# Performance work log

Hardware: AMD Instinct MI355X
Metric: run time of the kernel (lower is better)

## Reference

```python
import jax, jax.numpy as jnp
import numpy as np


def pairwise_distance(x):
    # x: [B,N,F] -> squared euclidean distance matrix [B,N,N]
    sq = jnp.sum(x * x, axis=-1)
    d = sq[:, :, None] + sq[:, None, :] - 2.0 * jnp.einsum('bnd,bmd->bnm', x, x)
    return jnp.maximum(d, 0.0)


def knn_adjacency(dist, k):
    # keep the k nearest neighbors of each point (binary adjacency)
    B, N, _ = dist.shape
    idx = jax.lax.top_k(-dist, k)[1]  # [B,N,k]
    A = jnp.zeros((B, N, N), dist.dtype)
    return A.at[jnp.arange(B)[:, None, None], jnp.arange(N)[None, :, None], idx].set(1.0)


def get_laplacian(A):
    # normalized graph Laplacian L = I - D^{-1/2} A D^{-1/2}
    d = jnp.sum(A, axis=-1)
    dinv = jnp.where(d > 0, 1.0 / jnp.sqrt(jnp.maximum(d, 1e-12)), 0.0)
    An = A * dinv[:, :, None] * dinv[:, None, :]
    return jnp.eye(A.shape[-1], dtype=A.dtype)[None] - An


def cheb_conv(x, L, W, b, K):
    # DenseChebConv: Chebyshev recurrence T0=x, T1=Lx, Tk=2L T_{k-1}-T_{k-2};
    # concat along features then dense projection. x:[B,N,Fin], W:[K*Fin,Fout]
    xs = [x]
    if K > 1:
        xs.append(jnp.einsum('bnm,bmf->bnf', L, x))
    for _ in range(2, K):
        xs.append(2.0 * jnp.einsum('bnm,bmf->bnf', L, xs[-1]) - xs[-2])
    xk = jnp.concatenate(xs, axis=-1)
    return jnp.einsum('bnf,fo->bno', xk, W) + b


def segment_max(out, idx):
    # fused replacement of the per-batch/per-cluster python loops:
    # out:[B,N,F], idx:[B,R,S] -> max-pooled cluster features [B,R,F]
    B = out.shape[0]
    g = out[jnp.arange(B)[:, None, None], idx]  # [B,R,S,F]
    return jnp.max(g, axis=2)


def setup_inputs():
    key = jax.random.key(0)
    ks = jax.random.split(key, 12)
    B, N, R, S, P = 32, 1024, 64, 16, 55
    inp = {}
    inp['x'] = jax.random.normal(ks[0], (B, N, 7), jnp.float32)
    inp['x2'] = jax.random.normal(ks[1], (B, N, 3), jnp.float32)
    inp['laplacian_Reeb'] = jax.random.normal(ks[2], (B, R, R), jnp.float32)
    inp['W1'] = jax.random.normal(ks[3], (3 * 7, 64), jnp.float32) * 0.1
    inp['b1'] = jnp.zeros((64,), jnp.float32)
    inp['W_reeb'] = jax.random.normal(ks[4], (6 * 64, 256), jnp.float32) * 0.05
    inp['b_reeb'] = jnp.zeros((256,), jnp.float32)
    inp['W_fps'] = jax.random.normal(ks[5], (6 * 64, 256), jnp.float32) * 0.05
    inp['b_fps'] = jnp.zeros((256,), jnp.float32)
    inp['fc1_w'] = jax.random.normal(ks[6], (512, 256), jnp.float32) * 0.05
    inp['fc1_b'] = jnp.zeros((256,), jnp.float32)
    inp['fc3_w'] = jax.random.normal(ks[7], (256, 40), jnp.float32) * 0.05
    inp['fc3_b'] = jnp.zeros((40,), jnp.float32)
    inp['sccs'] = jax.random.randint(ks[8], (B, R, S), 0, N)
    inp['sccs_fps'] = jax.random.randint(ks[9], (B, P, N), 0, N)
    inp['k'] = 30
    inp['batch_size'] = B
    inp['num_points'] = N
    return inp


def reference(x, x2, laplacian_Reeb, W1, b1, W_reeb, b_reeb, W_fps, b_fps,
              fc1_w, fc1_b, fc3_w, fc3_b, sccs, sccs_fps, k, batch_size, num_points):
    sg = jax.lax.stop_gradient
    # point-cloud kNN Laplacian (torch.no_grad in original)
    L = sg(get_laplacian(knn_adjacency(pairwise_distance(x), k)))
    out = jax.nn.relu(cheb_conv(x, L, W1, b1, 3))  # [B,N,64]
    reg1 = jnp.sum(jnp.einsum('bnf,bnm,bmg->bfg', out, L, out) ** 2)
    # Reeb-graph segment max pooling (no_grad in original)
    V_reeb = sg(segment_max(out, sccs))  # [B,R,64]
    L_reeb = sg(laplacian_Reeb)
    out_reeb = jax.nn.relu(cheb_conv(V_reeb, L_reeb, W_reeb, b_reeb, 6))  # [B,R,256]
    reg2 = jnp.sum(jnp.einsum('bnf,bnm,bmg->bfg', out_reeb, L_reeb, out_reeb) ** 2)
    # FPS cluster max pooling (no_grad in original)
    V_fps = sg(segment_max(out, sccs_fps))  # [B,55,64]
    L_fps = sg(get_laplacian(pairwise_distance(V_fps)))
    out_fps = jax.nn.relu(cheb_conv(V_fps, L_fps, W_fps, b_fps, 6))  # [B,55,256]
    reg3 = jnp.sum(jnp.einsum('bnf,bnm,bmg->bfg', out_fps, L_fps, out_fps) ** 2)
    feat = jnp.concatenate([jnp.max(out_reeb, axis=1), jnp.max(out_fps, axis=1)], axis=1)  # [B,512]
    h = jax.nn.relu(feat @ fc1_w + fc1_b)
    logits = h @ fc3_w + fc3_b  # [B,40]
    regs = jnp.stack([reg1, reg2, reg3,
                      jnp.sum(fc1_w[:, 0] ** 2), fc1_b[0] ** 2,
                      jnp.sum(fc3_w[:, 0] ** 2), fc3_b[0] ** 2])
    return logits, regs
```

## Files before the change

### kernel.cpp

```cpp
#include <hip/hip_runtime.h>
#include <math.h>

#define BN 32
#define NP 1024
#define KNN 30
#define NR 64
#define NFPS 55

__device__ __forceinline__ float lap_s() {
    const float dv = 1.0f / sqrtf(30.0f);
    return dv * dv;
}

__device__ __forceinline__ float dist7(const float4& xiA, const float4& xiB,
                                       float sqi, const float4& ca, const float4& cb) {
#pragma clang fp contract(off)
    float dot = xiA.x * ca.x;
    dot = fmaf(xiA.y, ca.y, dot);
    dot = fmaf(xiA.z, ca.z, dot);
    dot = fmaf(xiA.w, ca.w, dot);
    dot = fmaf(xiB.x, cb.x, dot);
    dot = fmaf(xiB.y, cb.y, dot);
    dot = fmaf(xiB.z, cb.z, dot);
    float r = sqi + cb.w;
    r = r - 2.f * dot;
    return fmaxf(r, 0.f);
}

__global__ __launch_bounds__(256) void k_knn(const float* __restrict__ x,
                                             int* __restrict__ knn,
                                             float* __restrict__ xs1,
                                             const float* __restrict__ fc1_w,
                                             const float* __restrict__ fc1_b,
                                             const float* __restrict__ fc3_w,
                                             const float* __restrict__ fc3_b,
                                             float* __restrict__ regs) {
    __shared__ float xls[NP * 8];
    __shared__ float vals[4 * KNN * 64];
    __shared__ float Tm[4 * 64];
    __shared__ int   Pk[4 * 64];
    int b = blockIdx.x;
    int t = threadIdx.x;
    int ln = t & 63, wv = t >> 6;

    if (b == 0 && blockIdx.y == 0) {
        float* r1 = vals;
        float* r2 = vals + 256;
        float s1 = 0.f;
        for (int i = t; i < 512; i += 256) { float v = fc1_w[(size_t)i * 256]; s1 += v * v; }
        float v2 = fc3_w[(size_t)t * 40];
        r1[t] = s1; r2[t] = v2 * v2;
        __syncthreads();
        for (int st = 128; st > 0; st >>= 1) {
            if (t < st) { r1[t] += r1[t + st]; r2[t] += r2[t + st]; }
            __syncthreads();
        }
        if (t == 0) {
            regs[0] = 0.f; regs[1] = 0.f; regs[2] = 0.f;
            regs[3] = r1[0];
            regs[4] = fc1_b[0] * fc1_b[0];
            regs[5] = r2[0];
            regs[6] = fc3_b[0] * fc3_b[0];
        }
        __syncthreads();
    }

    const float* xb = x + (size_t)b * NP * 7;
    for (int q = t; q < NP * 8; q += 256) {
        int r = q >> 3, d = q & 7;
        xls[q] = (d < 7) ? xb[r * 7 + d] : 0.f;
    }
    __syncthreads();
    for (int r = t; r < NP; r += 256) {
        float s = 0.f;
#pragma unroll
        for (int d = 0; d < 7; ++d) { float v = xls[r * 8 + d]; s += v * v; }
        xls[r * 8 + 7] = s;
    }
    __syncthreads();

    int grow = blockIdx.y * 64 + ln;
    float4 xiA = *(const float4*)&xls[grow * 8];
    float4 xiB = *(const float4*)&xls[grow * 8 + 4];
    float sqi = xiB.w;

    float bd[KNN];
#pragma unroll
    for (int q = 0; q < KNN; ++q) bd[q] = __builtin_inff();
    int jbase = wv * 256;
    for (int jc = 0; jc < 256; jc += 4) {
        const float* p = &xls[(jbase + jc) * 8];
        float4 a0 = *(const float4*)(p +  0), b0 = *(const float4*)(p +  4);
        float4 a1 = *(const float4*)(p +  8), b1 = *(const float4*)(p + 12);
        float4 a2 = *(const float4*)(p + 16), b2 = *(const float4*)(p + 20);
        float4 a3 = *(const float4*)(p + 24), b3 = *(const float4*)(p + 28);
        float d0 = dist7(xiA, xiB, sqi, a0, b0);
        float d1 = dist7(xiA, xiB, sqi, a1, b1);
        float d2 = dist7(xiA, xiB, sqi, a2, b2);
        float d3 = dist7(xiA, xiB, sqi, a3, b3);
#pragma unroll
        for (int q = KNN - 1; q >= 1; --q) bd[q] = __builtin_amdgcn_fmed3f(bd[q - 1], d0, bd[q]);
        bd[0] = fminf(bd[0], d0);
#pragma unroll
        for (int q = KNN - 1; q >= 1; --q) bd[q] = __builtin_amdgcn_fmed3f(bd[q - 1], d1, bd[q]);
        bd[0] = fminf(bd[0], d1);
#pragma unroll
        for (int q = KNN - 1; q >= 1; --q) bd[q] = __builtin_amdgcn_fmed3f(bd[q - 1], d2, bd[q]);
        bd[0] = fminf(bd[0], d2);
#pragma unroll
        for (int q = KNN - 1; q >= 1; --q) bd[q] = __builtin_amdgcn_fmed3f(bd[q - 1], d3, bd[q]);
        bd[0] = fminf(bd[0], d3);
    }
#pragma unroll
    for (int q = 0; q < KNN; ++q) vals[wv * (KNN * 64) + q * 64 + ln] = bd[q];
    __syncthreads();

    if (t < 64) {
        const float inf = __builtin_inff();
        float h0 = vals[0 * 1920 + t];
        float h1 = vals[1 * 1920 + t];
        float h2 = vals[2 * 1920 + t];
        float h3 = vals[3 * 1920 + t];
        int p0 = 0, p1 = 0, p2 = 0, p3 = 0;
        for (int s = 0; s < KNN; ++s) {
            float best = h0; int bw = 0;
            if (h1 < best) { best = h1; bw = 1; }
            if (h2 < best) { best = h2; bw = 2; }
            if (h3 < best) { best = h3; bw = 3; }
            if (bw == 0)      { ++p0; h0 = (p0 < KNN) ? vals[0 * 1920 + p0 * 64 + t] : inf; }
            else if (bw == 1) { ++p1; h1 = (p1 < KNN) ? vals[1 * 1920 + p1 * 64 + t] : inf; }
            else if (bw == 2) { ++p2; h2 = (p2 < KNN) ? vals[2 * 1920 + p2 * 64 + t] : inf; }
            else              { ++p3; h3 = (p3 < KNN) ? vals[3 * 1920 + p3 * 64 + t] : inf; }
        }
        int bacc = 0;
        int tks[4] = {p0, p1, p2, p3};
#pragma unroll
        for (int w = 0; w < 4; ++w) {
            int tk = tks[w];
            float T; int need;
            if (tk == 0) { T = -__builtin_inff(); need = 0; }
            else {
                T = vals[w * 1920 + (tk - 1) * 64 + t];
                need = 1;
                for (int q = tk - 2; q >= 0; --q) {
                    if (vals[w * 1920 + q * 64 + t] == T) ++need; else break;
                }
            }
            Tm[w * 64 + t] = T;
            Pk[w * 64 + t] = bacc | (need << 8) | (tk << 16);
            bacc += tk;
        }
    }
    __syncthreads();

    float Tw = Tm[wv * 64 + ln];
    int pk = Pk[wv * 64 + ln];
    int base = pk & 255, need = (pk >> 8) & 255, tk = pk >> 16;
    int* kout = knn + ((size_t)b * NP + grow) * KNN;
    float n0 = 0.f, n1 = 0.f, n2 = 0.f, n3 = 0.f, n4 = 0.f, n5 = 0.f, n6 = 0.f;
    int cs = 0, ct = 0;
    for (int jc = 0; jc < 256; jc += 4) {
        const float* p = &xls[(jbase + jc) * 8];
        float4 a0 = *(const float4*)(p +  0), b0 = *(const float4*)(p +  4);
        float4 a1 = *(const float4*)(p +  8), b1 = *(const float4*)(p + 12);
        float4 a2 = *(const float4*)(p + 16), b2 = *(const float4*)(p + 20);
        float4 a3 = *(const float4*)(p + 24), b3 = *(const float4*)(p + 28);
        float d0 = dist7(xiA, xiB, sqi, a0, b0);
        float d1 = dist7(xiA, xiB, sqi, a1, b1);
        float d2 = dist7(xiA, xiB, sqi, a2, b2);
        float d3 = dist7(xiA, xiB, sqi, a3, b3);
#pragma unroll
        for (int u = 0; u < 4; ++u) {
            float dist = (u == 0) ? d0 : (u == 1) ? d1 : (u == 2) ? d2 : d3;
            const float4& ca = (u == 0) ? a0 : (u == 1) ? a1 : (u == 2) ? a2 : a3;
            const float4& cb = (u == 0) ? b0 : (u == 1) ? b1 : (u == 2) ? b2 : b3;
            bool lt = dist < Tw;
            bool eq = (dist == Tw) && (ct < need);
            if ((lt || eq) && (cs + ct < tk)) {
                kout[base + cs + ct] = jbase + jc + u;
                cs += lt ? 1 : 0;
                ct += eq ? 1 : 0;
                n0 += ca.x; n1 += ca.y; n2 += ca.z; n3 += ca.w;
                n4 += cb.x; n5 += cb.y; n6 += cb.z;
            }
        }
    }
    for (int q = cs + ct; q < tk; ++q) kout[base + q] = grow;
    float* nsb = vals;
    nsb[wv * 448 + 0 * 64 + ln] = n0;
    nsb[wv * 448 + 1 * 64 + ln] = n1;
    nsb[wv * 448 + 2 * 64 + ln] = n2;
    nsb[wv * 448 + 3 * 64 + ln] = n3;
    nsb[wv * 448 + 4 * 64 + ln] = n4;
    nsb[wv * 448 + 5 * 64 + ln] = n5;
    nsb[wv * 448 + 6 * 64 + ln] = n6;
    __syncthreads();
    for (int u = t; u < 448; u += 256) {
        int d = u >> 6, rl = u & 63;
        float tot = nsb[d * 64 + rl] + nsb[448 + d * 64 + rl]
                  + nsb[896 + d * 64 + rl] + nsb[1344 + d * 64 + rl];
        int gr = blockIdx.y * 64 + rl;
        xs1[((size_t)b * NP + gr) * 7 + d] = xls[gr * 8 + d] - lap_s() * tot;
    }
}

__global__ __launch_bounds__(256) void k_out(const float* __restrict__ x,
                                             const float* __restrict__ xs1,
                                             const int* __restrict__ knn,
                                             const float* __restrict__ W1,
                                             const float* __restrict__ b1,
                                             float* __restrict__ out) {
    __shared__ float x1s[NP * 7];
    __shared__ float x0s[128 * 7];
    __shared__ float fr[128 * 21];
    __shared__ float W1s[21 * 64];
    __shared__ float b1s[64];
    int b = blockIdx.x;
    int rbase = blockIdx.y * 128;
    int t = threadIdx.x;
    for (int q = t; q < NP * 7; q += 256) x1s[q] = xs1[(size_t)b * NP * 7 + q];
    for (int q = t; q < 128 * 7; q += 256) x0s[q] = x[(size_t)b * NP * 7 + (size_t)rbase * 7 + q];
    for (int q = t; q < 21 * 64; q += 256) W1s[q] = W1[q];
    if (t < 64) b1s[t] = b1[t];
    __syncthreads();
    if (t < 128) {
        int i = rbase + t;
        float f[21];
#pragma unroll
        for (int d = 0; d < 7; ++d) { f[d] = x0s[t * 7 + d]; f[7 + d] = x1s[i * 7 + d]; }
        float ns[7] = {0.f, 0.f, 0.f, 0.f, 0.f, 0.f, 0.f};
        const int* kn = knn + ((size_t)b * NP + i) * KNN;
        for (int q = 0; q < KNN; ++q) {
            int j = kn[q];
#pragma unroll
            for (int d = 0; d < 7; ++d) ns[d] += x1s[j * 7 + d];
        }
        const float s = lap_s();
#pragma unroll
        for (int d = 0; d < 7; ++d) f[14 + d] = 2.f * (f[7 + d] - s * ns[d]) - f[d];
#pragma unroll
        for (int d = 0; d < 21; ++d) fr[t * 21 + d] = f[d];
    }
    __syncthreads();
    int o = t & 63, g = t >> 6;
    for (int m = 0; m < 32; ++m) {
        int r = g * 32 + m;
        float acc = b1s[o];
#pragma unroll
        for (int d = 0; d < 21; ++d) acc += fr[r * 21 + d] * W1s[d * 64 + o];
        out[((size_t)b * NP + rbase + r) * 64 + o] = fmaxf(acc, 0.f);
    }
}

__global__ __launch_bounds__(256) void k_z1v(const float* __restrict__ out,
                                             const int* __restrict__ knn,
                                             const int* __restrict__ sccs,
                                             const int* __restrict__ sccs_fps,
                                             float* __restrict__ Z1,
                                             float* __restrict__ Vr,
                                             float* __restrict__ Vf) {
    __shared__ int idxs[1024];
    __shared__ float red[256];
    int b = blockIdx.x, y = blockIdx.y;
    int t = threadIdx.x;
    const float* ob = out + (size_t)b * NP * 64;
    if (y < 256) {
        int i = y * 4 + (t >> 6);
        int f = t & 63;
        const int* kn = knn + ((size_t)b * NP + i) * KNN;
        float sum = 0.f;
        for (int q = 0; q < KNN; ++q) sum += ob[(size_t)kn[q] * 64 + f];
        Z1[((size_t)b * NP + i) * 64 + f] = ob[(size_t)i * 64 + f] - lap_s() * sum;
    } else if (y < 272) {
        int r = (y - 256) * 4 + (t >> 6);
        int f = t & 63;
        const int* sc = sccs + ((size_t)b * NR + r) * 16;
        float m = -__builtin_inff();
        for (int q = 0; q < 16; ++q) m = fmaxf(m, ob[(size_t)sc[q] * 64 + f]);
        Vr[((size_t)b * NR + r) * 64 + f] = m;
    } else {
        int p = y - 272;
        const int* sp = sccs_fps + ((size_t)b * NFPS + p) * 1024;
        for (int q = t; q < 1024; q += 256) idxs[q] = sp[q];
        __syncthreads();
        int f = t & 63, sc = t >> 6;
        float m = -__builtin_inff();
        for (int s = sc; s < 1024; s += 4) m = fmaxf(m, ob[(size_t)idxs[s] * 64 + f]);
        red[t] = m; __syncthreads();
        if (sc == 0) {
            m = fmaxf(fmaxf(red[f], red[64 + f]), fmaxf(red[128 + f], red[192 + f]));
            Vf[((size_t)b * NFPS + p) * 64 + f] = m;
        }
    }
}

__global__ __launch_bounds__(256) void k_t1_lfps(const float* __restrict__ out,
                                                 const float* __restrict__ Z1,
                                                 const float* __restrict__ Vfps,
                                                 float* __restrict__ regs,
                                                 float* __restrict__ Lf) {
    __shared__ float buf[8448];
    int b = blockIdx.x, y = blockIdx.y;
    int t = threadIdx.x;
    if (y < 2) {
        float* os = buf;
        float* zs = buf + 4096;
        float* red = buf + 8192;
        int f0 = y * 32;
        int fl = t >> 3;
        int gb = (t & 7) * 8;
        float acc[8];
#pragma unroll
        for (int q = 0; q < 8; ++q) acc[q] = 0.f;
        for (int c = 0; c < 16; ++c) {
            const float* ob = out + ((size_t)b * NP + c * 64) * 64;
            const float* zb = Z1 + ((size_t)b * NP + c * 64) * 64;
            for (int q = t; q < 64 * 64; q += 256) { os[q] = ob[q]; zs[q] = zb[q]; }
            __syncthreads();
            for (int n = 0; n < 64; ++n) {
                float a = os[n * 64 + f0 + fl];
#pragma unroll
                for (int q = 0; q < 8; ++q) acc[q] += a * zs[n * 64 + gb + q];
            }
            __syncthreads();
        }
        float loc = 0.f;
#pragma unroll
        for (int q = 0; q < 8; ++q) loc += acc[q] * acc[q];
        red[t] = loc; __syncthreads();
        for (int st = 128; st > 0; st >>= 1) { if (t < st) red[t] += red[t + st]; __syncthreads(); }
        if (t == 0) atomicAdd(&regs[0], red[0]);
    } else {
        float* Vs = buf;
        float* sq = buf + 3520;
        float* dist = buf + 3584;
        float* dinv = buf + 6609;
        for (int q = t; q < NFPS * 64; q += 256) Vs[q] = Vfps[(size_t)b * NFPS * 64 + q];
        __syncthreads();
        if (t < NFPS) {
            float s = 0.f;
            for (int f = 0; f < 64; ++f) { float v = Vs[t * 64 + f]; s += v * v; }
            sq[t] = s;
        }
        __syncthreads();
        for (int q = t; q < NFPS * NFPS; q += 256) {
            int i = q / NFPS, j = q % NFPS;
            float dot = 0.f;
            for (int f = 0; f < 64; ++f) dot += Vs[i * 64 + f] * Vs[j * 64 + f];
            dist[q] = fmaxf(sq[i] + sq[j] - 2.f * dot, 0.f);
        }
        __syncthreads();
        if (t < NFPS) {
            float s = 0.f;
            for (int j = 0; j < NFPS; ++j) s += dist[t * NFPS + j];
            dinv[t] = (s > 0.f) ? 1.0f / sqrtf(fmaxf(s, 1e-12f)) : 0.f;
        }
        __syncthreads();
        for (int q = t; q < NFPS * NFPS; q += 256) {
            int i = q / NFPS, j = q % NFPS;
            Lf[(size_t)b * NFPS * NFPS + q] = ((i == j) ? 1.f : 0.f) - dist[q] * dinv[i] * dinv[j];
        }
    }
}

template<int N>
__device__ __forceinline__ void cheb_impl(const float* __restrict__ L,
                                          const float* __restrict__ V,
                                          const float* __restrict__ W,
                                          const float* __restrict__ bias,
                                          float* __restrict__ out,
                                          float* __restrict__ Z,
                                          float* Ls, float* bA, float* bB, float* Ws,
                                          int b, int sl) {
    constexpr int NPAD = (N + 3) & ~3;
    int t = threadIdx.x;
    int c0 = (t & 15) * 4;
    int r0 = (t >> 4) * 4;

    for (int q = t; q < 64 * 64; q += 256) { Ls[q] = 0.f; bA[q] = 0.f; bB[q] = 0.f; }
    __syncthreads();
    for (int q = t; q < N * N; q += 256) {
        int r = q / N, m = q % N;
        Ls[r * 64 + m] = L[(size_t)b * N * N + q];
    }
    for (int q = t; q < N * 64; q += 256) bA[q] = V[(size_t)b * N * 64 + q];
    {
        const float* Wk = W + sl * 64;
        for (int q = t; q < 64 * 64; q += 256) Ws[q] = Wk[(q >> 6) * 256 + (q & 63)];
    }
    float4 a4[4];
    {
        float4 bv = *(const float4*)&bias[sl * 64 + c0];
#pragma unroll
        for (int i = 0; i < 4; ++i) a4[i] = bv;
    }
    __syncthreads();

    auto accum = [&](const float* xb) {
#pragma unroll 2
        for (int m = 0; m < 64; m += 4) {
            float4 xv[4], wv[4];
#pragma unroll
            for (int i = 0; i < 4; ++i) xv[i] = *(const float4*)&xb[(r0 + i) * 64 + m];
#pragma unroll
            for (int mm = 0; mm < 4; ++mm) wv[mm] = *(const float4*)&Ws[(m + mm) * 64 + c0];
#pragma unroll
            for (int i = 0; i < 4; ++i) {
                float xi0 = xv[i].x, xi1 = xv[i].y, xi2 = xv[i].z, xi3 = xv[i].w;
                a4[i].x += xi0 * wv[0].x; a4[i].y += xi0 * wv[0].y; a4[i].z += xi0 * wv[0].z; a4[i].w += xi0 * wv[0].w;
                a4[i].x += xi1 * wv[1].x; a4[i].y += xi1 * wv[1].y; a4[i].z += xi1 * wv[1].z; a4[i].w += xi1 * wv[1].w;
                a4[i].x += xi2 * wv[2].x; a4[i].y += xi2 * wv[2].y; a4[i].z += xi2 * wv[2].z; a4[i].w += xi2 * wv[2].w;
                a4[i].x += xi3 * wv[3].x; a4[i].y += xi3 * wv[3].y; a4[i].z += xi3 * wv[3].z; a4[i].w += xi3 * wv[3].w;
            }
        }
    };
    auto chebmm = [&](const float* src, float* dst, bool first) {
        float4 acc[4];
#pragma unroll
        for (int i = 0; i < 4; ++i) acc[i] = make_float4(0.f, 0.f, 0.f, 0.f);
#pragma unroll 2
        for (int m = 0; m < NPAD; m += 4) {
            float4 sv[4], lv[4];
#pragma unroll
            for (int mm = 0; mm < 4; ++mm) sv[mm] = *(const float4*)&src[(m + mm) * 64 + c0];
#pragma unroll
            for (int i = 0; i < 4; ++i) lv[i] = *(const float4*)&Ls[(r0 + i) * 64 + m];
#pragma unroll
            for (int i = 0; i < 4; ++i) {
                float l0 = lv[i].x, l1 = lv[i].y, l2 = lv[i].z, l3 = lv[i].w;
                acc[i].x += l0 * sv[0].x; acc[i].y += l0 * sv[0].y; acc[i].z += l0 * sv[0].z; acc[i].w += l0 * sv[0].w;
                acc[i].x += l1 * sv[1].x; acc[i].y += l1 * sv[1].y; acc[i].z += l1 * sv[1].z; acc[i].w += l1 * sv[1].w;
                acc[i].x += l2 * sv[2].x; acc[i].y += l2 * sv[2].y; acc[i].z += l2 * sv[2].z; acc[i].w += l2 * sv[2].w;
                acc[i].x += l3 * sv[3].x; acc[i].y += l3 * sv[3].y; acc[i].z += l3 * sv[3].z; acc[i].w += l3 * sv[3].w;
            }
        }
#pragma unroll
        for (int i = 0; i < 4; ++i) {
            if (r0 + i < N) {
                float4* d = (float4*)&dst[(r0 + i) * 64 + c0];
                if (first) *d = acc[i];
                else {
                    float4 od = *d;
                    *d = make_float4(2.f * acc[i].x - od.x, 2.f * acc[i].y - od.y,
                                     2.f * acc[i].z - od.z, 2.f * acc[i].w - od.w);
                }
            }
        }
    };
    auto loadW = [&](int k) {
        const float* Wk = W + (size_t)k * 64 * 256 + sl * 64;
        for (int q = t; q < 64 * 64; q += 256) Ws[q] = Wk[(q >> 6) * 256 + (q & 63)];
    };

    accum(bA);                 __syncthreads();
    chebmm(bA, bB, true);      loadW(1);  __syncthreads();
    accum(bB);                 __syncthreads();
    chebmm(bB, bA, false);     loadW(2);  __syncthreads();
    accum(bA);                 __syncthreads();
    chebmm(bA, bB, false);     loadW(3);  __syncthreads();
    accum(bB);                 __syncthreads();
    chebmm(bB, bA, false);     loadW(4);  __syncthreads();
    accum(bA);                 __syncthreads();
    chebmm(bA, bB, false);     loadW(5);  __syncthreads();
    accum(bB);                 __syncthreads();

    float* ob = out + (size_t)b * N * 256 + sl * 64;
#pragma unroll
    for (int i = 0; i < 4; ++i) {
        if (r0 + i < N) {
            float4 v = make_float4(fmaxf(a4[i].x, 0.f), fmaxf(a4[i].y, 0.f),
                                   fmaxf(a4[i].z, 0.f), fmaxf(a4[i].w, 0.f));
            *(float4*)&bA[(r0 + i) * 64 + c0] = v;
            *(float4*)&ob[(size_t)(r0 + i) * 256 + c0] = v;
        }
    }
    __syncthreads();
    {
        float4 acc[4];
#pragma unroll
        for (int i = 0; i < 4; ++i) acc[i] = make_float4(0.f, 0.f, 0.f, 0.f);
#pragma unroll 2
        for (int m = 0; m < NPAD; m += 4) {
            float4 sv[4], lv[4];
#pragma unroll
            for (int mm = 0; mm < 4; ++mm) sv[mm] = *(const float4*)&bA[(m + mm) * 64 + c0];
#pragma unroll
            for (int i = 0; i < 4; ++i) lv[i] = *(const float4*)&Ls[(r0 + i) * 64 + m];
#pragma unroll
            for (int i = 0; i < 4; ++i) {
                float l0 = lv[i].x, l1 = lv[i].y, l2 = lv[i].z, l3 = lv[i].w;
                acc[i].x += l0 * sv[0].x; acc[i].y += l0 * sv[0].y; acc[i].z += l0 * sv[0].z; acc[i].w += l0 * sv[0].w;
                acc[i].x += l1 * sv[1].x; acc[i].y += l1 * sv[1].y; acc[i].z += l1 * sv[1].z; acc[i].w += l1 * sv[1].w;
                acc[i].x += l2 * sv[2].x; acc[i].y += l2 * sv[2].y; acc[i].z += l2 * sv[2].z; acc[i].w += l2 * sv[2].w;
                acc[i].x += l3 * sv[3].x; acc[i].y += l3 * sv[3].y; acc[i].z += l3 * sv[3].z; acc[i].w += l3 * sv[3].w;
            }
        }
        float* zb = Z + (size_t)b * N * 256 + sl * 64;
#pragma unroll
        for (int i = 0; i < 4; ++i)
            if (r0 + i < N) *(float4*)&zb[(size_t)(r0 + i) * 256 + c0] = acc[i];
    }
}

__global__ __launch_bounds__(256) void k_cheb_fused(
        const float* __restrict__ Lr, const float* __restrict__ Vr,
        const float* __restrict__ Wr, const float* __restrict__ br,
        float* __restrict__ outR, float* __restrict__ Zr,
        const float* __restrict__ Lf, const float* __restrict__ Vf,
        const float* __restrict__ Wf, const float* __restrict__ bf,
        float* __restrict__ outP, float* __restrict__ Zf) {
    __shared__ float Ls[64 * 64];
    __shared__ float bA[64 * 64];
    __shared__ float bB[64 * 64];
    __shared__ float Ws[64 * 64];
    int b = blockIdx.x, y = blockIdx.y;
    if (y < 4) cheb_impl<NR>(Lr, Vr, Wr, br, outR, Zr, Ls, bA, bB, Ws, b, y);
    else       cheb_impl<NFPS>(Lf, Vf, Wf, bf, outP, Zf, Ls, bA, bB, Ws, b, y - 4);
}

template<int N>
__device__ __forceinline__ void treg_impl(const float* __restrict__ out,
                                          const float* __restrict__ Z,
                                          float* __restrict__ reg,
                                          float* zs, float* os, float* red, int y) {
    int b = blockIdx.x;
    int f0 = (y >> 1) * 32;
    int g0 = (y & 1) * 128;
    int t = threadIdx.x;
    for (int q = t; q < N * 128; q += 256) {
        int r = q >> 7, gl = q & 127;
        zs[q] = Z[(size_t)b * N * 256 + r * 256 + g0 + gl];
    }
    for (int q = t; q < N * 32; q += 256) {
        int r = q >> 5, f = q & 31;
        os[q] = out[(size_t)b * N * 256 + r * 256 + f0 + f];
    }
    __syncthreads();
    int fl = t >> 3;
    int gb = (t & 7) * 16;
    float accv[16];
#pragma unroll
    for (int q = 0; q < 16; ++q) accv[q] = 0.f;
    for (int n = 0; n < N; ++n) {
        float a = os[n * 32 + fl];
        const float* zr = zs + n * 128 + gb;
#pragma unroll
        for (int q = 0; q < 16; ++q) accv[q] += a * zr[q];
    }
    float loc = 0.f;
#pragma unroll
    for (int q = 0; q < 16; ++q) loc += accv[q] * accv[q];
    red[t] = loc; __syncthreads();
    for (int st = 128; st > 0; st >>= 1) { if (t < st) red[t] += red[t + st]; __syncthreads(); }
    if (t == 0) atomicAdd(reg, red[0]);
}

__global__ __launch_bounds__(256) void k_treg_tail(
        const float* __restrict__ outR, const float* __restrict__ Zr,
        const float* __restrict__ outP, const float* __restrict__ Zf,
        const float* __restrict__ fc1_w, const float* __restrict__ fc1_b,
        const float* __restrict__ fc3_w, const float* __restrict__ fc3_b,
        float* __restrict__ regs, float* __restrict__ logits) {
    __shared__ float zs[64 * 128];
    __shared__ float os[64 * 32];
    __shared__ float red[256];
    int y = blockIdx.y;
    if (y < 16) treg_impl<NR>(outR, Zr, regs + 1, zs, os, red, y);
    else if (y < 32) treg_impl<NFPS>(outP, Zf, regs + 2, zs, os, red, y - 16);
    else {
        int b = blockIdx.x, t = threadIdx.x;
        float* feat = zs;
        float* h = os;
        float m = -__builtin_inff();
        for (int r = 0; r < NR; ++r) m = fmaxf(m, outR[((size_t)b * NR + r) * 256 + t]);
        feat[t] = m;
        m = -__builtin_inff();
        for (int p = 0; p < NFPS; ++p) m = fmaxf(m, outP[((size_t)b * NFPS + p) * 256 + t]);
        feat[256 + t] = m;
        __syncthreads();
        float a = fc1_b[t];
        for (int i = 0; i < 512; ++i) a += feat[i] * fc1_w[(size_t)i * 256 + t];
        h[t] = fmaxf(a, 0.f);
        __syncthreads();
        if (t < 40) {
            float a2 = fc3_b[t];
            for (int i = 0; i < 256; ++i) a2 += h[i] * fc3_w[(size_t)i * 40 + t];
            logits[(size_t)b * 40 + t] = a2;
        }
    }
}

extern "C" void kernel_launch(void* const* d_in, const int* in_sizes, int n_in,
                              void* d_out, int out_size, void* d_ws, size_t ws_size,
                              hipStream_t stream) {
    const float* x      = (const float*)d_in[0];
    const float* L_reeb = (const float*)d_in[2];
    const float* W1     = (const float*)d_in[3];
    const float* b1     = (const float*)d_in[4];
    const float* W_reeb = (const float*)d_in[5];
    const float* b_reeb = (const float*)d_in[6];
    const float* W_fps  = (const float*)d_in[7];
    const float* b_fps  = (const float*)d_in[8];
    const float* fc1_w  = (const float*)d_in[9];
    const float* fc1_b  = (const float*)d_in[10];
    const float* fc3_w  = (const float*)d_in[11];
    const float* fc3_b  = (const float*)d_in[12];
    const int*   sccs   = (const int*)d_in[13];
    const int*   sccs_f = (const int*)d_in[14];

    float* outv = (float*)d_out;
    float* regs = outv + 1280;

    char* w = (char*)d_ws;
    size_t off = 0;
    auto alloc = [&](size_t bytes) { void* p = w + off; off = (off + bytes + 255) & ~(size_t)255; return p; };
    int*   knn   = (int*)  alloc((size_t)BN * NP * KNN * 4);
    float* xs1   = (float*)alloc((size_t)BN * NP * 7 * 4);
    float* outF  = (float*)alloc((size_t)BN * NP * 64 * 4);
    float* Z1    = (float*)alloc((size_t)BN * NP * 64 * 4);
    float* Vreeb = (float*)alloc((size_t)BN * NR * 64 * 4);
    float* outRb = (float*)alloc((size_t)BN * NR * 256 * 4);
    float* Z2    = (float*)alloc((size_t)BN * NR * 256 * 4);
    float* Vfps  = (float*)alloc((size_t)BN * NFPS * 64 * 4);
    float* Lfps  = (float*)alloc((size_t)BN * NFPS * NFPS * 4);
    float* outP  = (float*)alloc((size_t)BN * NFPS * 256 * 4);
    float* Z3    = (float*)alloc((size_t)BN * NFPS * 256 * 4);

    k_knn<<<dim3(BN, NP / 64), 256, 0, stream>>>(x, knn, xs1,
                                                 fc1_w, fc1_b, fc3_w, fc3_b, regs);
    k_out<<<dim3(BN, 8), 256, 0, stream>>>(x, xs1, knn, W1, b1, outF);
    k_z1v<<<dim3(BN, 256 + 16 + NFPS), 256, 0, stream>>>(outF, knn, sccs, sccs_f,
                                                         Z1, Vreeb, Vfps);
    k_t1_lfps<<<dim3(BN, 3), 256, 0, stream>>>(outF, Z1, Vfps, regs, Lfps);
    k_cheb_fused<<<dim3(BN, 8), 256, 0, stream>>>(L_reeb, Vreeb, W_reeb, b_reeb, outRb, Z2,
                                                  Lfps, Vfps, W_fps, b_fps, outP, Z3);
    k_treg_tail<<<dim3(BN, 33), 256, 0, stream>>>(outRb, Z2, outP, Z3,
                                                  fc1_w, fc1_b, fc3_w, fc3_b, regs, outv);
}
```

Baseline: 387.4 us.

## Rebalance mid-pipeline kernels, prefetch merge candidates, and halve k_out tile

Restages the cross-kernel schedule. Reeb Chebyshev now runs alongside the t1 regularizer and FPS Laplacian build, and FPS Chebyshev runs alongside the Reeb regularizer, so independent work shares launches instead of waiting on a strict chain. The weight-norm regs init moves out of the kNN kernel into an extra block of k_out, whose row tile is halved to 64 to launch more blocks. The 4-way merge in k_knn now prefetches the next candidate and tracks tie run lengths inline, replacing the backward rescan. The risks are larger shared-memory footprints in the fused kernels and load imbalance between the heterogeneous blocks of one launch.

```diff
diff --git a/kernel.cpp b/kernel.cpp
--- a/kernel.cpp
+++ b/kernel.cpp
@@ -29,12 +29,7 @@
 
 __global__ __launch_bounds__(256) void k_knn(const float* __restrict__ x,
                                              int* __restrict__ knn,
-                                             float* __restrict__ xs1,
-                                             const float* __restrict__ fc1_w,
-                                             const float* __restrict__ fc1_b,
-                                             const float* __restrict__ fc3_w,
-                                             const float* __restrict__ fc3_b,
-                                             float* __restrict__ regs) {
+                                             float* __restrict__ xs1) {
     __shared__ float xls[NP * 8];
     __shared__ float vals[4 * KNN * 64];
     __shared__ float Tm[4 * 64];
@@ -42,28 +37,6 @@
     int b = blockIdx.x;
     int t = threadIdx.x;
     int ln = t & 63, wv = t >> 6;
-
-    if (b == 0 && blockIdx.y == 0) {
-        float* r1 = vals;
-        float* r2 = vals + 256;
-        float s1 = 0.f;
-        for (int i = t; i < 512; i += 256) { float v = fc1_w[(size_t)i * 256]; s1 += v * v; }
-        float v2 = fc3_w[(size_t)t * 40];
-        r1[t] = s1; r2[t] = v2 * v2;
-        __syncthreads();
-        for (int st = 128; st > 0; st >>= 1) {
-            if (t < st) { r1[t] += r1[t + st]; r2[t] += r2[t + st]; }
-            __syncthreads();
-        }
-        if (t == 0) {
-            regs[0] = 0.f; regs[1] = 0.f; regs[2] = 0.f;
-            regs[3] = r1[0];
-            regs[4] = fc1_b[0] * fc1_b[0];
-            regs[5] = r2[0];
-            regs[6] = fc3_b[0] * fc3_b[0];
-        }
-        __syncthreads();
-    }
 
     const float* xb = x + (size_t)b * NP * 7;
     for (int q = t; q < NP * 8; q += 256) {
@@ -117,39 +90,37 @@
 
     if (t < 64) {
         const float inf = __builtin_inff();
-        float h0 = vals[0 * 1920 + t];
-        float h1 = vals[1 * 1920 + t];
-        float h2 = vals[2 * 1920 + t];
-        float h3 = vals[3 * 1920 + t];
+        float h0 = vals[0 * 1920 + t], n0v = vals[0 * 1920 + 64 + t];
+        float h1 = vals[1 * 1920 + t], n1v = vals[1 * 1920 + 64 + t];
+        float h2 = vals[2 * 1920 + t], n2v = vals[2 * 1920 + 64 + t];
+        float h3 = vals[3 * 1920 + t], n3v = vals[3 * 1920 + 64 + t];
         int p0 = 0, p1 = 0, p2 = 0, p3 = 0;
+        float lv0 = inf, lv1 = inf, lv2 = inf, lv3 = inf;
+        int r0 = 0, r1 = 0, r2 = 0, r3 = 0;
         for (int s = 0; s < KNN; ++s) {
             float best = h0; int bw = 0;
             if (h1 < best) { best = h1; bw = 1; }
             if (h2 < best) { best = h2; bw = 2; }
             if (h3 < best) { best = h3; bw = 3; }
-            if (bw == 0)      { ++p0; h0 = (p0 < KNN) ? vals[0 * 1920 + p0 * 64 + t] : inf; }
-            else if (bw == 1) { ++p1; h1 = (p1 < KNN) ? vals[1 * 1920 + p1 * 64 + t] : inf; }
-            else if (bw == 2) { ++p2; h2 = (p2 < KNN) ? vals[2 * 1920 + p2 * 64 + t] : inf; }
-            else              { ++p3; h3 = (p3 < KNN) ? vals[3 * 1920 + p3 * 64 + t] : inf; }
-        }
-        int bacc = 0;
-        int tks[4] = {p0, p1, p2, p3};
-#pragma unroll
-        for (int w = 0; w < 4; ++w) {
-            int tk = tks[w];
-            float T; int need;
-            if (tk == 0) { T = -__builtin_inff(); need = 0; }
-            else {
-                T = vals[w * 1920 + (tk - 1) * 64 + t];
-                need = 1;
-                for (int q = tk - 2; q >= 0; --q) {
-                    if (vals[w * 1920 + q * 64 + t] == T) ++need; else break;
-                }
+            if (bw == 0) {
+                r0 = (best == lv0) ? r0 + 1 : 1; lv0 = best;
+                ++p0; h0 = n0v; n0v = (p0 + 1 < KNN) ? vals[0 * 1920 + (p0 + 1) * 64 + t] : inf;
+            } else if (bw == 1) {
+                r1 = (best == lv1) ? r1 + 1 : 1; lv1 = best;
+                ++p1; h1 = n1v; n1v = (p1 + 1 < KNN) ? vals[1 * 1920 + (p1 + 1) * 64 + t] : inf;
+            } else if (bw == 2) {
+                r2 = (best == lv2) ? r2 + 1 : 1; lv2 = best;
+                ++p2; h2 = n2v; n2v = (p2 + 1 < KNN) ? vals[2 * 1920 + (p2 + 1) * 64 + t] : inf;
+            } else {
+                r3 = (best == lv3) ? r3 + 1 : 1; lv3 = best;
+                ++p3; h3 = n3v; n3v = (p3 + 1 < KNN) ? vals[3 * 1920 + (p3 + 1) * 64 + t] : inf;
             }
-            Tm[w * 64 + t] = T;
-            Pk[w * 64 + t] = bacc | (need << 8) | (tk << 16);
-            bacc += tk;
-        }
+        }
+        Tm[0 * 64 + t] = lv0; Pk[0 * 64 + t] = 0 | (r0 << 8) | (p0 << 16);
+        int bacc = p0;
+        Tm[1 * 64 + t] = lv1; Pk[1 * 64 + t] = bacc | (r1 << 8) | (p1 << 16); bacc += p1;
+        Tm[2 * 64 + t] = lv2; Pk[2 * 64 + t] = bacc | (r2 << 8) | (p2 << 16); bacc += p2;
+        Tm[3 * 64 + t] = lv3; Pk[3 * 64 + t] = bacc | (r3 << 8) | (p3 << 16);
     }
     __syncthreads();
 
@@ -209,21 +180,48 @@
                                              const int* __restrict__ knn,
                                              const float* __restrict__ W1,
                                              const float* __restrict__ b1,
-                                             float* __restrict__ out) {
+                                             float* __restrict__ out,
+                                             const float* __restrict__ fc1_w,
+                                             const float* __restrict__ fc1_b,
+                                             const float* __restrict__ fc3_w,
+                                             const float* __restrict__ fc3_b,
+                                             float* __restrict__ regs) {
     __shared__ float x1s[NP * 7];
-    __shared__ float x0s[128 * 7];
-    __shared__ float fr[128 * 21];
+    __shared__ float x0s[64 * 7];
+    __shared__ float fr[64 * 21];
     __shared__ float W1s[21 * 64];
     __shared__ float b1s[64];
-    int b = blockIdx.x;
-    int rbase = blockIdx.y * 128;
+    int b = blockIdx.x, y = blockIdx.y;
     int t = threadIdx.x;
+    if (y == 16) {
+        if (b != 0) return;
+        float* r1 = x1s;
+        float* r2 = x1s + 256;
+        float s1 = 0.f;
+        for (int i = t; i < 512; i += 256) { float v = fc1_w[(size_t)i * 256]; s1 += v * v; }
+        float v2 = fc3_w[(size_t)t * 40];
+        r1[t] = s1; r2[t] = v2 * v2;
+        __syncthreads();
+        for (int st = 128; st > 0; st >>= 1) {
+            if (t < st) { r1[t] += r1[t + st]; r2[t] += r2[t + st]; }
+            __syncthreads();
+        }
+        if (t == 0) {
+            regs[0] = 0.f; regs[1] = 0.f; regs[2] = 0.f;
+            regs[3] = r1[0];
+            regs[4] = fc1_b[0] * fc1_b[0];
+            regs[5] = r2[0];
+            regs[6] = fc3_b[0] * fc3_b[0];
+        }
+        return;
+    }
+    int rbase = y * 64;
     for (int q = t; q < NP * 7; q += 256) x1s[q] = xs1[(size_t)b * NP * 7 + q];
-    for (int q = t; q < 128 * 7; q += 256) x0s[q] = x[(size_t)b * NP * 7 + (size_t)rbase * 7 + q];
+    for (int q = t; q < 64 * 7; q += 256) x0s[q] = x[(size_t)b * NP * 7 + (size_t)rbase * 7 + q];
     for (int q = t; q < 21 * 64; q += 256) W1s[q] = W1[q];
     if (t < 64) b1s[t] = b1[t];
     __syncthreads();
-    if (t < 128) {
+    if (t < 64) {
         int i = rbase + t;
         float f[21];
 #pragma unroll
@@ -243,8 +241,8 @@
     }
     __syncthreads();
     int o = t & 63, g = t >> 6;
-    for (int m = 0; m < 32; ++m) {
-        int r = g * 32 + m;
+    for (int m = 0; m < 16; ++m) {
+        int r = g * 16 + m;
         float acc = b1s[o];
 #pragma unroll
         for (int d = 0; d < 21; ++d) acc += fr[r * 21 + d] * W1s[d * 64 + o];
@@ -294,72 +292,73 @@
     }
 }
 
-__global__ __launch_bounds__(256) void k_t1_lfps(const float* __restrict__ out,
-                                                 const float* __restrict__ Z1,
-                                                 const float* __restrict__ Vfps,
-                                                 float* __restrict__ regs,
-                                                 float* __restrict__ Lf) {
-    __shared__ float buf[8448];
-    int b = blockIdx.x, y = blockIdx.y;
+__device__ __forceinline__ void t1_impl(const float* __restrict__ out,
+                                        const float* __restrict__ Z1,
+                                        float* __restrict__ regs,
+                                        float* buf, int y) {
+    int b = blockIdx.x;
     int t = threadIdx.x;
-    if (y < 2) {
-        float* os = buf;
-        float* zs = buf + 4096;
-        float* red = buf + 8192;
-        int f0 = y * 32;
-        int fl = t >> 3;
-        int gb = (t & 7) * 8;
-        float acc[8];
-#pragma unroll
-        for (int q = 0; q < 8; ++q) acc[q] = 0.f;
-        for (int c = 0; c < 16; ++c) {
-            const float* ob = out + ((size_t)b * NP + c * 64) * 64;
-            const float* zb = Z1 + ((size_t)b * NP + c * 64) * 64;
-            for (int q = t; q < 64 * 64; q += 256) { os[q] = ob[q]; zs[q] = zb[q]; }
-            __syncthreads();
-            for (int n = 0; n < 64; ++n) {
-                float a = os[n * 64 + f0 + fl];
-#pragma unroll
-                for (int q = 0; q < 8; ++q) acc[q] += a * zs[n * 64 + gb + q];
-            }
-            __syncthreads();
-        }
-        float loc = 0.f;
-#pragma unroll
-        for (int q = 0; q < 8; ++q) loc += acc[q] * acc[q];
-        red[t] = loc; __syncthreads();
-        for (int st = 128; st > 0; st >>= 1) { if (t < st) red[t] += red[t + st]; __syncthreads(); }
-        if (t == 0) atomicAdd(&regs[0], red[0]);
-    } else {
-        float* Vs = buf;
-        float* sq = buf + 3520;
-        float* dist = buf + 3584;
-        float* dinv = buf + 6609;
-        for (int q = t; q < NFPS * 64; q += 256) Vs[q] = Vfps[(size_t)b * NFPS * 64 + q];
+    float* os = buf;
+    float* zs = buf + 4096;
+    float* red = buf + 8192;
+    int f0 = y * 32;
+    int fl = t >> 3;
+    int gb = (t & 7) * 8;
+    float acc[8];
+#pragma unroll
+    for (int q = 0; q < 8; ++q) acc[q] = 0.f;
+    for (int c = 0; c < 16; ++c) {
+        const float* ob = out + ((size_t)b * NP + c * 64) * 64;
+        const float* zb = Z1 + ((size_t)b * NP + c * 64) * 64;
+        for (int q = t; q < 64 * 64; q += 256) { os[q] = ob[q]; zs[q] = zb[q]; }
         __syncthreads();
-        if (t < NFPS) {
-            float s = 0.f;
-            for (int f = 0; f < 64; ++f) { float v = Vs[t * 64 + f]; s += v * v; }
-            sq[t] = s;
+        for (int n = 0; n < 64; ++n) {
+            float a = os[n * 64 + f0 + fl];
+#pragma unroll
+            for (int q = 0; q < 8; ++q) acc[q] += a * zs[n * 64 + gb + q];
         }
         __syncthreads();
-        for (int q = t; q < NFPS * NFPS; q += 256) {
-            int i = q / NFPS, j = q % NFPS;
-            float dot = 0.f;
-            for (int f = 0; f < 64; ++f) dot += Vs[i * 64 + f] * Vs[j * 64 + f];
-            dist[q] = fmaxf(sq[i] + sq[j] - 2.f * dot, 0.f);
-        }
-        __syncthreads();
-        if (t < NFPS) {
-            float s = 0.f;
-            for (int j = 0; j < NFPS; ++j) s += dist[t * NFPS + j];
-            dinv[t] = (s > 0.f) ? 1.0f / sqrtf(fmaxf(s, 1e-12f)) : 0.f;
-        }
-        __syncthreads();
-        for (int q = t; q < NFPS * NFPS; q += 256) {
-            int i = q / NFPS, j = q % NFPS;
-            Lf[(size_t)b * NFPS * NFPS + q] = ((i == j) ? 1.f : 0.f) - dist[q] * dinv[i] * dinv[j];
-        }
+    }
+    float loc = 0.f;
+#pragma unroll
+    for (int q = 0; q < 8; ++q) loc += acc[q] * acc[q];
+    red[t] = loc; __syncthreads();
+    for (int st = 128; st > 0; st >>= 1) { if (t < st) red[t] += red[t + st]; __syncthreads(); }
+    if (t == 0) atomicAdd(&regs[0], red[0]);
+}
+
+__device__ __forceinline__ void lfps_impl(const float* __restrict__ Vfps,
+                                          float* __restrict__ Lf, float* buf) {
+    int b = blockIdx.x;
+    int t = threadIdx.x;
+    float* Vs = buf;
+    float* sq = buf + 3520;
+    float* dist = buf + 3584;
+    float* dinv = buf + 6609;
+    for (int q = t; q < NFPS * 64; q += 256) Vs[q] = Vfps[(size_t)b * NFPS * 64 + q];
+    __syncthreads();
+    if (t < NFPS) {
+        float s = 0.f;
+        for (int f = 0; f < 64; ++f) { float v = Vs[t * 64 + f]; s += v * v; }
+        sq[t] = s;
+    }
+    __syncthreads();
+    for (int q = t; q < NFPS * NFPS; q += 256) {
+        int i = q / NFPS, j = q % NFPS;
+        float dot = 0.f;
+        for (int f = 0; f < 64; ++f) dot += Vs[i * 64 + f] * Vs[j * 64 + f];
+        dist[q] = fmaxf(sq[i] + sq[j] - 2.f * dot, 0.f);
+    }
+    __syncthreads();
+    if (t < NFPS) {
+        float s = 0.f;
+        for (int j = 0; j < NFPS; ++j) s += dist[t * NFPS + j];
+        dinv[t] = (s > 0.f) ? 1.0f / sqrtf(fmaxf(s, 1e-12f)) : 0.f;
+    }
+    __syncthreads();
+    for (int q = t; q < NFPS * NFPS; q += 256) {
+        int i = q / NFPS, j = q % NFPS;
+        Lf[(size_t)b * NFPS * NFPS + q] = ((i == j) ? 1.f : 0.f) - dist[q] * dinv[i] * dinv[j];
     }
 }
 
@@ -502,22 +501,6 @@
     }
 }
 
-__global__ __launch_bounds__(256) void k_cheb_fused(
-        const float* __restrict__ Lr, const float* __restrict__ Vr,
-        const float* __restrict__ Wr, const float* __restrict__ br,
-        float* __restrict__ outR, float* __restrict__ Zr,
-        const float* __restrict__ Lf, const float* __restrict__ Vf,
-        const float* __restrict__ Wf, const float* __restrict__ bf,
-        float* __restrict__ outP, float* __restrict__ Zf) {
-    __shared__ float Ls[64 * 64];
-    __shared__ float bA[64 * 64];
-    __shared__ float bB[64 * 64];
-    __shared__ float Ws[64 * 64];
-    int b = blockIdx.x, y = blockIdx.y;
-    if (y < 4) cheb_impl<NR>(Lr, Vr, Wr, br, outR, Zr, Ls, bA, bB, Ws, b, y);
-    else       cheb_impl<NFPS>(Lf, Vf, Wf, bf, outP, Zf, Ls, bA, bB, Ws, b, y - 4);
-}
-
 template<int N>
 __device__ __forceinline__ void treg_impl(const float* __restrict__ out,
                                           const float* __restrict__ Z,
@@ -555,22 +538,49 @@
     if (t == 0) atomicAdd(reg, red[0]);
 }
 
-__global__ __launch_bounds__(256) void k_treg_tail(
+__global__ __launch_bounds__(256) void k_mid1(
+        const float* __restrict__ out, const float* __restrict__ Z1,
+        const float* __restrict__ Vfps, float* __restrict__ regs,
+        float* __restrict__ Lf,
+        const float* __restrict__ Lr, const float* __restrict__ Vr,
+        const float* __restrict__ Wr, const float* __restrict__ br,
+        float* __restrict__ outR, float* __restrict__ Zr) {
+    __shared__ float smem[16384];
+    int y = blockIdx.y;
+    if (y < 2)       t1_impl(out, Z1, regs, smem, y);
+    else if (y == 2) lfps_impl(Vfps, Lf, smem);
+    else cheb_impl<NR>(Lr, Vr, Wr, br, outR, Zr,
+                       smem, smem + 4096, smem + 8192, smem + 12288,
+                       blockIdx.x, y - 3);
+}
+
+__global__ __launch_bounds__(256) void k_mid2(
+        const float* __restrict__ Lf, const float* __restrict__ Vf,
+        const float* __restrict__ Wf, const float* __restrict__ bf,
+        float* __restrict__ outP, float* __restrict__ Zf,
         const float* __restrict__ outR, const float* __restrict__ Zr,
+        float* __restrict__ regs) {
+    __shared__ float smem[16384];
+    int y = blockIdx.y;
+    if (y < 4) cheb_impl<NFPS>(Lf, Vf, Wf, bf, outP, Zf,
+                               smem, smem + 4096, smem + 8192, smem + 12288,
+                               blockIdx.x, y);
+    else treg_impl<NR>(outR, Zr, regs + 1, smem, smem + 8192, smem + 10240, y - 4);
+}
+
+__global__ __launch_bounds__(256) void k_fin(
         const float* __restrict__ outP, const float* __restrict__ Zf,
+        const float* __restrict__ outR,
         const float* __restrict__ fc1_w, const float* __restrict__ fc1_b,
         const float* __restrict__ fc3_w, const float* __restrict__ fc3_b,
         float* __restrict__ regs, float* __restrict__ logits) {
-    __shared__ float zs[64 * 128];
-    __shared__ float os[64 * 32];
-    __shared__ float red[256];
+    __shared__ float smem[10496];
     int y = blockIdx.y;
-    if (y < 16) treg_impl<NR>(outR, Zr, regs + 1, zs, os, red, y);
-    else if (y < 32) treg_impl<NFPS>(outP, Zf, regs + 2, zs, os, red, y - 16);
+    if (y < 16) treg_impl<NFPS>(outP, Zf, regs + 2, smem, smem + 8192, smem + 10240, y);
     else {
         int b = blockIdx.x, t = threadIdx.x;
-        float* feat = zs;
-        float* h = os;
+        float* feat = smem;
+        float* h = smem + 8192;
         float m = -__builtin_inff();
         for (int r = 0; r < NR; ++r) m = fmaxf(m, outR[((size_t)b * NR + r) * 256 + t]);
         feat[t] = m;
@@ -626,14 +636,15 @@
     float* outP  = (float*)alloc((size_t)BN * NFPS * 256 * 4);
     float* Z3    = (float*)alloc((size_t)BN * NFPS * 256 * 4);
 
-    k_knn<<<dim3(BN, NP / 64), 256, 0, stream>>>(x, knn, xs1,
-                                                 fc1_w, fc1_b, fc3_w, fc3_b, regs);
-    k_out<<<dim3(BN, 8), 256, 0, stream>>>(x, xs1, knn, W1, b1, outF);
+    k_knn<<<dim3(BN, NP / 64), 256, 0, stream>>>(x, knn, xs1);
+    k_out<<<dim3(BN, 17), 256, 0, stream>>>(x, xs1, knn, W1, b1, outF,
+                                            fc1_w, fc1_b, fc3_w, fc3_b, regs);
     k_z1v<<<dim3(BN, 256 + 16 + NFPS), 256, 0, stream>>>(outF, knn, sccs, sccs_f,
                                                          Z1, Vreeb, Vfps);
-    k_t1_lfps<<<dim3(BN, 3), 256, 0, stream>>>(outF, Z1, Vfps, regs, Lfps);
-    k_cheb_fused<<<dim3(BN, 8), 256, 0, stream>>>(L_reeb, Vreeb, W_reeb, b_reeb, outRb, Z2,
-                                                  Lfps, Vfps, W_fps, b_fps, outP, Z3);
-    k_treg_tail<<<dim3(BN, 33), 256, 0, stream>>>(outRb, Z2, outP, Z3,
-                                                  fc1_w, fc1_b, fc3_w, fc3_b, regs, outv);
-}
+    k_mid1<<<dim3(BN, 7), 256, 0, stream>>>(outF, Z1, Vfps, regs, Lfps,
+                                            L_reeb, Vreeb, W_reeb, b_reeb, outRb, Z2);
+    k_mid2<<<dim3(BN, 20), 256, 0, stream>>>(Lfps, Vfps, W_fps, b_fps, outP, Z3,
+                                             outRb, Z2, regs);
+    k_fin<<<dim3(BN, 17), 256, 0, stream>>>(outP, Z3, outRb,
+                                            fc1_w, fc1_b, fc3_w, fc3_b, regs, outv);
+}
```

Result: no change. 385.3 us (-0.5%).
